# Optimization experiments

Hardware: AMD Instinct MI355X
Metric: run time of the kernel (lower is better)

The kernel has to match this reference:

```python
import jax, jax.numpy as jnp
import numpy as np

B, S, H = 16, 1024, 4
QD, KD, VD = 128, 256, 256


def setup_inputs() -> dict:
    key = jax.random.key(0)
    ks = jax.random.split(key, 12)
    s = 0.02
    return {
        "query": jax.random.normal(ks[0], (B, S, QD), jnp.float32),
        "key": jax.random.normal(ks[1], (B, S, KD), jnp.float32),
        "value": jax.random.normal(ks[2], (B, S, VD), jnp.float32),
        "Wq": jax.random.normal(ks[3], (QD, KD * H), jnp.float32) * s,
        "bq": jnp.zeros((KD * H,), jnp.float32),
        "Wk": jax.random.normal(ks[4], (KD, KD * H), jnp.float32) * s,
        "bk": jnp.zeros((KD * H,), jnp.float32),
        "Wv": jax.random.normal(ks[5], (VD, VD * H), jnp.float32) * s,
        "bv": jnp.zeros((VD * H,), jnp.float32),
        "Wo": jax.random.normal(ks[6], (VD * H, 8 * VD), jnp.float32) * s,
        "bo": jnp.zeros((8 * VD,), jnp.float32),
        "W1": jax.random.normal(ks[7], (8 * VD, 128), jnp.float32) * s,
        "b1": jnp.zeros((128,), jnp.float32),
        "random_len": S,
    }


def reference(query, key, value, Wq, bq, Wk, bk, Wv, bv, Wo, bo, W1, b1, random_len):
    b = query.shape[0]
    # flat view [B, S, H*D] -> [B, H, S, D], exactly matching torch .view semantics
    tq = (query @ Wq + bq).reshape(b, H, -1, KD)
    tk = (key @ Wk + bk).reshape(b, H, -1, KD)
    tv = (value @ Wv + bv).reshape(b, H, -1, VD)
    # NOTE: original has NO 1/sqrt(d) scaling
    scores = jnp.einsum("bhqd,bhkd->bhqk", tq, tk)  # [B,H,S,S]
    attn = jax.nn.softmax(scores, axis=-1)
    attended = jnp.einsum("bhqk,bhkd->bhqd", attn, tv)  # [B,H,S,VD]
    attended = attended.reshape(b, -1, VD * H)  # [B,S,H*VD]
    out = attended @ Wo + bo  # [B,S,2048]
    out = out.mean(axis=1)  # [B,2048]
    out = out @ W1 + b1  # [B,128]
    return out, attn
```

## Files before the change

kernel.cpp:

```cpp
#include <hip/hip_runtime.h>
#include <hip/hip_bf16.h>

typedef _Float16 half_t;
typedef _Float16 half8 __attribute__((ext_vector_type(8)));
typedef _Float16 half4v __attribute__((ext_vector_type(4)));
typedef float floatx4 __attribute__((ext_vector_type(4)));

__global__ __launch_bounds__(256) void wtrans_kernel(const float* __restrict__ W,
                                                     half_t* __restrict__ Wt, int K, int N) {
  __shared__ float sm[32][33];
  int n0 = blockIdx.x * 32, k0 = blockIdx.y * 32;
  int x = threadIdx.x & 31, y0 = threadIdx.x >> 5;
#pragma unroll
  for (int yy = 0; yy < 4; ++yy) {
    int y = y0 + yy * 8;
    sm[y][x] = W[(size_t)(k0 + y) * N + n0 + x];
  }
  __syncthreads();
#pragma unroll
  for (int yy = 0; yy < 4; ++yy) {
    int y = y0 + yy * 8;
    Wt[(size_t)(n0 + y) * K + k0 + x] = (half_t)sm[x][y];
  }
}

template <bool AF32, bool BIAS>
__global__ __launch_bounds__(256) void gemm_nt(
    const float* __restrict__ Af, const half_t* __restrict__ Ah,
    const half_t* __restrict__ Bt, const float* __restrict__ bias,
    half_t* __restrict__ C, int K, int ldc,
    size_t aStrideZ, size_t bStrideZ, size_t cStrideZ) {
  __shared__ half_t sA[128 * 32];
  __shared__ half_t sB[128 * 32];
  const int t = threadIdx.x;
  const int m0 = blockIdx.x * 128;
  const int n0 = blockIdx.y * 128;
  const int z = blockIdx.z;
  const half_t* Bz = Bt + bStrideZ * (size_t)z;
  const int w = t >> 6, lane = t & 63;
  const int wm = w & 1, wn = w >> 1;
  const int lr = lane & 15, lk = lane >> 4;
  const int srow = t >> 2, sg = t & 3;

  floatx4 acc[4][4] = {};

  for (int k0 = 0; k0 < K; k0 += 32) {
    __syncthreads();
#pragma unroll
    for (int rep = 0; rep < 2; ++rep) {
      int row = srow + rep * 64;
      int goff = (sg ^ ((row >> 1) & 3)) * 8;
      half8 hv;
      if constexpr (AF32) {
        const float* p = Af + (size_t)(m0 + row) * K + k0 + sg * 8;
        float4 f0 = *(const float4*)p;
        float4 f1 = *(const float4*)(p + 4);
        hv[0] = (half_t)f0.x; hv[1] = (half_t)f0.y;
        hv[2] = (half_t)f0.z; hv[3] = (half_t)f0.w;
        hv[4] = (half_t)f1.x; hv[5] = (half_t)f1.y;
        hv[6] = (half_t)f1.z; hv[7] = (half_t)f1.w;
      } else {
        const half_t* p = Ah + aStrideZ * (size_t)z + (size_t)(m0 + row) * K + k0 + sg * 8;
        hv = *(const half8*)p;
      }
      *(half8*)&sA[row * 32 + goff] = hv;
      const half_t* q = Bz + (size_t)(n0 + row) * K + k0 + sg * 8;
      *(half8*)&sB[row * 32 + goff] = *(const half8*)q;
    }
    __syncthreads();
    half8 af[4], bf[4];
#pragma unroll
    for (int mt = 0; mt < 4; ++mt) {
      int row = wm * 64 + mt * 16 + lr;
      af[mt] = *(const half8*)&sA[row * 32 + ((lk ^ ((row >> 1) & 3)) * 8)];
    }
#pragma unroll
    for (int nt = 0; nt < 4; ++nt) {
      int row = wn * 64 + nt * 16 + lr;
      bf[nt] = *(const half8*)&sB[row * 32 + ((lk ^ ((row >> 1) & 3)) * 8)];
    }
#pragma unroll
    for (int mt = 0; mt < 4; ++mt)
#pragma unroll
      for (int nt = 0; nt < 4; ++nt)
        acc[mt][nt] = __builtin_amdgcn_mfma_f32_16x16x32_f16(bf[nt], af[mt], acc[mt][nt], 0, 0, 0);
  }

  half_t* Cz = C + cStrideZ * (size_t)z;
#pragma unroll
  for (int mt = 0; mt < 4; ++mt) {
    int m = m0 + wm * 64 + mt * 16 + lr;
#pragma unroll
    for (int nt = 0; nt < 4; ++nt) {
      int nb = n0 + wn * 64 + nt * 16 + lk * 4;
      floatx4 a = acc[mt][nt];
      half4v h;
      if constexpr (BIAS) {
        float4 bv = *(const float4*)&bias[nb];
        h[0] = (half_t)(a[0] + bv.x); h[1] = (half_t)(a[1] + bv.y);
        h[2] = (half_t)(a[2] + bv.z); h[3] = (half_t)(a[3] + bv.w);
      } else {
        h[0] = (half_t)a[0]; h[1] = (half_t)a[1];
        h[2] = (half_t)a[2]; h[3] = (half_t)a[3];
      }
      *(half4v*)&Cz[(size_t)m * ldc + nb] = h;
    }
  }
}

__global__ __launch_bounds__(256, 2) void fused_attn_kernel(
    const half_t* __restrict__ Tq, const half_t* __restrict__ Tk,
    float* __restrict__ attn, float* __restrict__ cs) {
  const int z = blockIdx.y;
  const int q0 = blockIdx.x * 32;
  const int t = threadIdx.x;
  const int w = t >> 6, lane = t & 63;
  const int lr = lane & 15, lk = lane >> 4;

  __shared__ half_t sQ[32 * 264];
  __shared__ float sRS[4][32];

  const half_t* Tqz = Tq + (size_t)z * 262144 + (size_t)q0 * 256;
  for (int c = t; c < 1024; c += 256) {
    int row = c >> 5, col8 = (c & 31) * 8;
    *(half8*)&sQ[row * 264 + col8] = *(const half8*)&Tqz[row * 256 + col8];
  }
  __syncthreads();

  const half_t* Tkz = Tk + (size_t)z * 262144;
  const int nb = w * 256;

  floatx4 acc[2][16] = {};
  for (int k0 = 0; k0 < 256; k0 += 32) {
    half8 af0 = *(const half8*)&sQ[lr * 264 + k0 + lk * 8];
    half8 af1 = *(const half8*)&sQ[(16 + lr) * 264 + k0 + lk * 8];
#pragma unroll
    for (int nt = 0; nt < 16; ++nt) {
      half8 bf = *(const half8*)&Tkz[(size_t)(nb + nt * 16 + lr) * 256 + k0 + lk * 8];
      acc[0][nt] = __builtin_amdgcn_mfma_f32_16x16x32_f16(bf, af0, acc[0][nt], 0, 0, 0);
      acc[1][nt] = __builtin_amdgcn_mfma_f32_16x16x32_f16(bf, af1, acc[1][nt], 0, 0, 0);
    }
  }

  float rs0 = 0.0f, rs1 = 0.0f;
#pragma unroll
  for (int nt = 0; nt < 16; ++nt) {
#pragma unroll
    for (int j = 0; j < 4; ++j) {
      float v0 = __expf(acc[0][nt][j]);
      float v1 = __expf(acc[1][nt][j]);
      acc[0][nt][j] = v0; acc[1][nt][j] = v1;
      rs0 += v0; rs1 += v1;
    }
  }
  rs0 += __shfl_xor(rs0, 16); rs0 += __shfl_xor(rs0, 32);
  rs1 += __shfl_xor(rs1, 16); rs1 += __shfl_xor(rs1, 32);
  if (lane < 16) { sRS[w][lane] = rs0; sRS[w][16 + lane] = rs1; }
  __syncthreads();
  float inv0 = 1.0f / (sRS[0][lr] + sRS[1][lr] + sRS[2][lr] + sRS[3][lr]);
  float inv1 = 1.0f / (sRS[0][16 + lr] + sRS[1][16 + lr] + sRS[2][16 + lr] + sRS[3][16 + lr]);

  float* attnz = attn + (size_t)z * 1048576;
  float* csz = cs + (size_t)z * 4096;
#pragma unroll
  for (int nt = 0; nt < 16; ++nt) {
    int n = nb + nt * 16 + lk * 4;
    float4 o0, o1;
    o0.x = acc[0][nt][0] * inv0; o0.y = acc[0][nt][1] * inv0;
    o0.z = acc[0][nt][2] * inv0; o0.w = acc[0][nt][3] * inv0;
    o1.x = acc[1][nt][0] * inv1; o1.y = acc[1][nt][1] * inv1;
    o1.z = acc[1][nt][2] * inv1; o1.w = acc[1][nt][3] * inv1;
    *(float4*)&attnz[(size_t)(q0 + lr) * 1024 + n] = o0;
    *(float4*)&attnz[(size_t)(q0 + 16 + lr) * 1024 + n] = o1;
    float c0 = o0.x + o1.x, c1 = o0.y + o1.y, c2 = o0.z + o1.z, c3 = o0.w + o1.w;
    c0 += __shfl_xor(c0, 4); c0 += __shfl_xor(c0, 8);
    c1 += __shfl_xor(c1, 4); c1 += __shfl_xor(c1, 8);
    c2 += __shfl_xor(c2, 4); c2 += __shfl_xor(c2, 8);
    c3 += __shfl_xor(c3, 4); c3 += __shfl_xor(c3, 8);
    if (lr < 4) {
      float* p = csz + (size_t)lr * 1024 + n;
      atomicAdd(p + 0, c0);
      atomicAdd(p + 1, c1);
      atomicAdd(p + 2, c2);
      atomicAdd(p + 3, c3);
    }
  }
}

__global__ __launch_bounds__(256) void abar_kernel(const float* __restrict__ cs,
                                                   const half_t* __restrict__ Tv,
                                                   float* __restrict__ abar) {
  int b = blockIdx.x, r = blockIdx.y, kc = blockIdx.z;
  int d = threadIdx.x;
  __shared__ float scs[4][128];
  for (int idx = d; idx < 512; idx += 256) {
    int h = idx >> 7, k = idx & 127;
    scs[h][k] = cs[(size_t)(b * 4 + h) * 4096 + (size_t)r * 1024 + kc * 128 + k];
  }
  __syncthreads();
  float acc = 0.0f;
  for (int h = 0; h < 4; ++h) {
    const half_t* tv = Tv + (size_t)(b * 4 + h) * 262144 + (size_t)kc * 32768 + d;
#pragma unroll 4
    for (int k = 0; k < 128; ++k)
      acc += scs[h][k] * (float)tv[(size_t)k * 256];
  }
  atomicAdd(&abar[b * 1024 + r * 256 + d], acc * (1.0f / 1024.0f));
}

__global__ __launch_bounds__(256) void bcomb_kernel(const float* __restrict__ bo,
                                                    const float* __restrict__ W1,
                                                    const float* __restrict__ b1,
                                                    float* __restrict__ bcomb) {
  int t = threadIdx.x;
  int j = t & 127, h = t >> 7;
  float acc = 0.0f;
  for (int k = h * 1024; k < h * 1024 + 1024; ++k)
    acc += bo[k] * W1[(size_t)k * 128 + j];
  __shared__ float sm[2][128];
  sm[h][j] = acc;
  __syncthreads();
  if (t < 128) bcomb[t] = sm[0][t] + sm[1][t] + b1[t];
}

__global__ __launch_bounds__(256) void final2_kernel(const float* __restrict__ abar,
                                                     const half_t* __restrict__ Wcomb,
                                                     const float* __restrict__ bcomb,
                                                     float* __restrict__ out) {
  int b = blockIdx.x, t = threadIdx.x;
  int j = t & 127, h = t >> 7;
  __shared__ float sa[1024];
  __shared__ float sm[2][128];
  for (int i = t; i < 1024; i += 256) sa[i] = abar[(size_t)b * 1024 + i];
  __syncthreads();
  float acc = 0.0f;
  for (int c = h * 512; c < h * 512 + 512; ++c)
    acc += sa[c] * (float)Wcomb[(size_t)c * 128 + j];
  sm[h][j] = acc;
  __syncthreads();
  if (t < 128) out[(size_t)b * 128 + t] = sm[0][t] + sm[1][t] + bcomb[t];
}

extern "C" void kernel_launch(void* const* d_in, const int* in_sizes, int n_in,
                              void* d_out, int out_size, void* d_ws, size_t ws_size,
                              hipStream_t stream) {
  const float* query = (const float*)d_in[0];
  const float* key   = (const float*)d_in[1];
  const float* value = (const float*)d_in[2];
  const float* Wq = (const float*)d_in[3];
  const float* bq = (const float*)d_in[4];
  const float* Wk = (const float*)d_in[5];
  const float* bk = (const float*)d_in[6];
  const float* Wv = (const float*)d_in[7];
  const float* bv = (const float*)d_in[8];
  const float* Wo = (const float*)d_in[9];
  const float* bo = (const float*)d_in[10];
  const float* W1 = (const float*)d_in[11];
  const float* b1 = (const float*)d_in[12];

  char* ws = (char*)d_ws;
  half_t* Tq   = (half_t*)(ws + 0);
  half_t* Tk   = (half_t*)(ws + 33554432);
  half_t* Tv   = (half_t*)(ws + 67108864);
  float*  cs   = (float*)(ws + 100663296);
  float*  abar = (float*)(ws + 101711872);
  half_t* Wqt  = (half_t*)(ws + 101777408);
  half_t* Wkt  = (half_t*)(ws + 102039552);
  half_t* Wvt  = (half_t*)(ws + 102563840);
  half_t* W1t   = (half_t*)(ws + 0);
  half_t* Wcomb = (half_t*)(ws + 524288);
  float*  bcomb = (float*)(ws + 786432);

  float* out  = (float*)d_out;
  float* attn = out + 2048;

  hipMemsetAsync(cs, 0, 1048576 + 65536, stream);

  wtrans_kernel<<<dim3(32, 4), 256, 0, stream>>>(Wq, Wqt, 128, 1024);
  wtrans_kernel<<<dim3(32, 8), 256, 0, stream>>>(Wk, Wkt, 256, 1024);
  wtrans_kernel<<<dim3(32, 8), 256, 0, stream>>>(Wv, Wvt, 256, 1024);

  gemm_nt<true, true><<<dim3(128, 8, 1), 256, 0, stream>>>(query, nullptr, Wqt, bq, Tq, 128, 1024, 0, 0, 0);
  gemm_nt<true, true><<<dim3(128, 8, 1), 256, 0, stream>>>(key,   nullptr, Wkt, bk, Tk, 256, 1024, 0, 0, 0);
  gemm_nt<true, true><<<dim3(128, 8, 1), 256, 0, stream>>>(value, nullptr, Wvt, bv, Tv, 256, 1024, 0, 0, 0);

  fused_attn_kernel<<<dim3(32, 64), 256, 0, stream>>>(Tq, Tk, attn, cs);

  wtrans_kernel<<<dim3(4, 64), 256, 0, stream>>>(W1, W1t, 2048, 128);
  gemm_nt<true, false><<<dim3(8, 1, 1), 256, 0, stream>>>(Wo, nullptr, W1t, nullptr, Wcomb, 2048, 128, 0, 0, 0);
  bcomb_kernel<<<1, 256, 0, stream>>>(bo, W1, b1, bcomb);

  abar_kernel<<<dim3(16, 4, 8), 256, 0, stream>>>(cs, Tv, abar);
  final2_kernel<<<16, 256, 0, stream>>>(abar, Wcomb, bcomb, out);
}
```

Baseline: 808.5 us.

## Stage K tiles through double-buffered swizzled LDS in the attention score kernel

Replaces the per-wave direct global loads of K fragments in the QK^T loop with a cooperative block-wide copy into a two-slot LDS buffer. The next 32-wide K chunk is prefetched into registers while MFMAs consume the current slot, using an XOR swizzle to avoid bank conflicts. The loop is reordered into 32 stages (4 row groups x 8 k-steps). The aim is to hide global load latency behind the matrix math. In exchange it adds 32 KB of LDS per block and a __syncthreads per stage, which may limit occupancy or add stalls.

```diff
diff --git a/kernel.cpp b/kernel.cpp
--- a/kernel.cpp
+++ b/kernel.cpp
@@ -116,8 +116,10 @@
   const int t = threadIdx.x;
   const int w = t >> 6, lane = t & 63;
   const int lr = lane & 15, lk = lane >> 4;
+  const int srow = t >> 2, sg = t & 3;
 
   __shared__ half_t sQ[32 * 264];
+  __shared__ half_t sK[2][256 * 32];
   __shared__ float sRS[4][32];
 
   const half_t* Tqz = Tq + (size_t)z * 262144 + (size_t)q0 * 256;
@@ -125,20 +127,55 @@
     int row = c >> 5, col8 = (c & 31) * 8;
     *(half8*)&sQ[row * 264 + col8] = *(const half8*)&Tqz[row * 256 + col8];
   }
-  __syncthreads();
 
   const half_t* Tkz = Tk + (size_t)z * 262144;
-  const int nb = w * 256;
+
+  half8 st[4];
+  {
+#pragma unroll
+    for (int rep = 0; rep < 4; ++rep) {
+      int sl = rep * 64 + srow;
+      int grow = rep * 256 + srow;
+      st[rep] = *(const half8*)&Tkz[(size_t)grow * 256 + ((sg ^ ((sl >> 1) & 3)) * 8)];
+    }
+#pragma unroll
+    for (int rep = 0; rep < 4; ++rep) {
+      int sl = rep * 64 + srow;
+      *(half8*)&sK[0][sl * 32 + sg * 8] = st[rep];
+    }
+  }
+  __syncthreads();
 
   floatx4 acc[2][16] = {};
-  for (int k0 = 0; k0 < 256; k0 += 32) {
-    half8 af0 = *(const half8*)&sQ[lr * 264 + k0 + lk * 8];
-    half8 af1 = *(const half8*)&sQ[(16 + lr) * 264 + k0 + lk * 8];
-#pragma unroll
-    for (int nt = 0; nt < 16; ++nt) {
-      half8 bf = *(const half8*)&Tkz[(size_t)(nb + nt * 16 + lr) * 256 + k0 + lk * 8];
-      acc[0][nt] = __builtin_amdgcn_mfma_f32_16x16x32_f16(bf, af0, acc[0][nt], 0, 0, 0);
-      acc[1][nt] = __builtin_amdgcn_mfma_f32_16x16x32_f16(bf, af1, acc[1][nt], 0, 0, 0);
+#pragma unroll
+  for (int s = 0; s < 32; ++s) {
+    const int cur = s & 1;
+    if (s + 1 < 32) {
+      const int gn = (s + 1) >> 3, k0n = (s + 1) & 7;
+#pragma unroll
+      for (int rep = 0; rep < 4; ++rep) {
+        int sl = rep * 64 + srow;
+        int grow = rep * 256 + gn * 64 + srow;
+        st[rep] = *(const half8*)&Tkz[(size_t)grow * 256 + k0n * 32 + ((sg ^ ((sl >> 1) & 3)) * 8)];
+      }
+    }
+    const int g = s >> 3, k0s = s & 7;
+    half8 af0 = *(const half8*)&sQ[lr * 264 + k0s * 32 + lk * 8];
+    half8 af1 = *(const half8*)&sQ[(16 + lr) * 264 + k0s * 32 + lk * 8];
+#pragma unroll
+    for (int l = 0; l < 4; ++l) {
+      int sl = w * 64 + l * 16 + lr;
+      half8 bf = *(const half8*)&sK[cur][sl * 32 + ((lk ^ ((sl >> 1) & 3)) * 8)];
+      acc[0][g * 4 + l] = __builtin_amdgcn_mfma_f32_16x16x32_f16(bf, af0, acc[0][g * 4 + l], 0, 0, 0);
+      acc[1][g * 4 + l] = __builtin_amdgcn_mfma_f32_16x16x32_f16(bf, af1, acc[1][g * 4 + l], 0, 0, 0);
+    }
+    if (s + 1 < 32) {
+#pragma unroll
+      for (int rep = 0; rep < 4; ++rep) {
+        int sl = rep * 64 + srow;
+        *(half8*)&sK[cur ^ 1][sl * 32 + sg * 8] = st[rep];
+      }
+      __syncthreads();
     }
   }
 
@@ -160,6 +197,7 @@
   float inv0 = 1.0f / (sRS[0][lr] + sRS[1][lr] + sRS[2][lr] + sRS[3][lr]);
   float inv1 = 1.0f / (sRS[0][16 + lr] + sRS[1][16 + lr] + sRS[2][16 + lr] + sRS[3][16 + lr]);
 
+  const int nb = w * 256;
   float* attnz = attn + (size_t)z * 1048576;
   float* csz = cs + (size_t)z * 4096;
 #pragma unroll
```

Result: faster. 735.9 us (-9.0%).

## Stage K tiles through LDS with async global_load_lds triple buffering

Applied to the files above, without the earlier changes.

The QK^T loop in the fused attention kernel no longer reads K straight from global memory into registers. Q and K tiles are now copied into LDS with direct global-to-LDS loads, using an XOR swizzle to avoid bank conflicts. K is staged through a three-slot ring buffer that prefetches two steps ahead, with vmcnt waits and barriers. The aim is to overlap K fetches with MFMA work and let the block's waves share K through LDS. In exchange it uses more LDS, which may reduce occupancy, and relies on hand-tuned waitcnt counts that must match the number of loads in flight.

```diff
diff --git a/kernel.cpp b/kernel.cpp
--- a/kernel.cpp
+++ b/kernel.cpp
@@ -5,6 +5,12 @@
 typedef _Float16 half8 __attribute__((ext_vector_type(8)));
 typedef _Float16 half4v __attribute__((ext_vector_type(4)));
 typedef float floatx4 __attribute__((ext_vector_type(4)));
+
+__device__ inline void gload16(const half_t* g, half_t* l) {
+  __builtin_amdgcn_global_load_lds(
+      (const __attribute__((address_space(1))) void*)g,
+      (__attribute__((address_space(3))) void*)l, 16, 0, 0);
+}
 
 __global__ __launch_bounds__(256) void wtrans_kernel(const float* __restrict__ W,
                                                      half_t* __restrict__ Wt, int K, int N) {
@@ -117,28 +123,66 @@
   const int w = t >> 6, lane = t & 63;
   const int lr = lane & 15, lk = lane >> 4;
 
-  __shared__ half_t sQ[32 * 264];
+  __shared__ half_t sQ[32 * 256];
+  __shared__ half_t sK[3][256 * 32];
   __shared__ float sRS[4][32];
 
   const half_t* Tqz = Tq + (size_t)z * 262144 + (size_t)q0 * 256;
-  for (int c = t; c < 1024; c += 256) {
-    int row = c >> 5, col8 = (c & 31) * 8;
-    *(half8*)&sQ[row * 264 + col8] = *(const half8*)&Tqz[row * 256 + col8];
-  }
-  __syncthreads();
-
   const half_t* Tkz = Tk + (size_t)z * 262144;
-  const int nb = w * 256;
+
+#pragma unroll
+  for (int r = 0; r < 4; ++r) {
+    int i = r * 256 + w * 64 + lane;
+    int row = i >> 5, j8 = i & 31;
+    gload16(Tqz + (size_t)row * 256 + ((j8 ^ (row & 7)) * 8), &sQ[(r * 256 + w * 64) * 8]);
+  }
+#pragma unroll
+  for (int sp = 0; sp < 2; ++sp) {
+#pragma unroll
+    for (int r = 0; r < 4; ++r) {
+      int i = r * 256 + w * 64 + lane;
+      int sl = i >> 2, kg = i & 3;
+      int grow = ((sl >> 6) << 8) + (sl & 63);
+      gload16(Tkz + (size_t)grow * 256 + sp * 32 + ((kg ^ ((sl >> 1) & 3)) * 8),
+              &sK[sp][(r * 256 + w * 64) * 8]);
+    }
+  }
 
   floatx4 acc[2][16] = {};
-  for (int k0 = 0; k0 < 256; k0 += 32) {
-    half8 af0 = *(const half8*)&sQ[lr * 264 + k0 + lk * 8];
-    half8 af1 = *(const half8*)&sQ[(16 + lr) * 264 + k0 + lk * 8];
-#pragma unroll
-    for (int nt = 0; nt < 16; ++nt) {
-      half8 bf = *(const half8*)&Tkz[(size_t)(nb + nt * 16 + lr) * 256 + k0 + lk * 8];
-      acc[0][nt] = __builtin_amdgcn_mfma_f32_16x16x32_f16(bf, af0, acc[0][nt], 0, 0, 0);
-      acc[1][nt] = __builtin_amdgcn_mfma_f32_16x16x32_f16(bf, af1, acc[1][nt], 0, 0, 0);
+#pragma unroll
+  for (int s = 0; s < 32; ++s) {
+    if (s < 31) {
+      asm volatile("s_waitcnt vmcnt(4)" ::: "memory");
+    } else {
+      asm volatile("s_waitcnt vmcnt(0)" ::: "memory");
+    }
+    __builtin_amdgcn_sched_barrier(0);
+    __builtin_amdgcn_s_barrier();
+
+    if (s + 2 < 32) {
+      const int sp = s + 2, g2 = sp >> 3, ks2 = sp & 7;
+      half_t* base = &sK[sp % 3][0];
+#pragma unroll
+      for (int r = 0; r < 4; ++r) {
+        int i = r * 256 + w * 64 + lane;
+        int sl = i >> 2, kg = i & 3;
+        int grow = ((sl >> 6) << 8) + g2 * 64 + (sl & 63);
+        gload16(Tkz + (size_t)grow * 256 + ks2 * 32 + ((kg ^ ((sl >> 1) & 3)) * 8),
+                base + (r * 256 + w * 64) * 8);
+      }
+    }
+
+    const int g = s >> 3, ks = s & 7;
+    const half_t* kb = &sK[s % 3][0];
+    const int j8 = ((ks * 4 + lk) ^ (lr & 7)) * 8;
+    half8 af0 = *(const half8*)&sQ[lr * 256 + j8];
+    half8 af1 = *(const half8*)&sQ[(16 + lr) * 256 + j8];
+#pragma unroll
+    for (int l = 0; l < 4; ++l) {
+      int sl = w * 64 + l * 16 + lr;
+      half8 bf = *(const half8*)&kb[sl * 32 + ((lk ^ ((sl >> 1) & 3)) * 8)];
+      acc[0][g * 4 + l] = __builtin_amdgcn_mfma_f32_16x16x32_f16(bf, af0, acc[0][g * 4 + l], 0, 0, 0);
+      acc[1][g * 4 + l] = __builtin_amdgcn_mfma_f32_16x16x32_f16(bf, af1, acc[1][g * 4 + l], 0, 0, 0);
     }
   }
 
@@ -160,6 +204,7 @@
   float inv0 = 1.0f / (sRS[0][lr] + sRS[1][lr] + sRS[2][lr] + sRS[3][lr]);
   float inv1 = 1.0f / (sRS[0][16 + lr] + sRS[1][16 + lr] + sRS[2][16 + lr] + sRS[3][16 + lr]);
 
+  const int nb = w * 256;
   float* attnz = attn + (size_t)z * 1048576;
   float* csz = cs + (size_t)z * 4096;
 #pragma unroll
```

New measurement: 712.8 us. -11.8%, faster.
